# Kernel optimization log

Measured on AMD Instinct MI355X. Metric: run time of the kernel, lower is better.

The kernel has to match this reference:

```python
import jax, jax.numpy as jnp
import numpy as np

N_NODES = 100000
N_EDGES = 1600000
INPUT_DIM = 128
HIDDEN = 128
OUTPUT_DIM = 2
NUM_LAYERS = 2
MAX_RECURSION = 10
TAU_THRESHOLD = 0.005


def setup_inputs() -> dict:
    key = jax.random.key(0)
    ks = jax.random.split(key, 16)
    s = 0.05
    x = jax.random.normal(ks[0], (N_NODES, INPUT_DIM), dtype=jnp.float32)
    edge_index = jax.random.randint(ks[1], (2, N_EDGES), 0, N_NODES, dtype=jnp.int64)
    W_in = jax.random.normal(ks[2], (HIDDEN, INPUT_DIM), dtype=jnp.float32) * s
    b_in = jax.random.normal(ks[3], (HIDDEN,), dtype=jnp.float32) * s
    Wd = jax.random.normal(ks[4], (NUM_LAYERS, HIDDEN, 2 * HIDDEN), dtype=jnp.float32) * s
    bd = jax.random.normal(ks[5], (NUM_LAYERS, HIDDEN), dtype=jnp.float32) * s
    Wt = jax.random.normal(ks[6], (1, HIDDEN), dtype=jnp.float32) * s
    bt = jax.random.normal(ks[7], (1,), dtype=jnp.float32) * s
    W_ih = jax.random.normal(ks[8], (3 * HIDDEN, HIDDEN), dtype=jnp.float32) * s
    W_hh = jax.random.normal(ks[9], (3 * HIDDEN, HIDDEN), dtype=jnp.float32) * s
    b_ih = jax.random.normal(ks[10], (3 * HIDDEN,), dtype=jnp.float32) * s
    b_hh = jax.random.normal(ks[11], (3 * HIDDEN,), dtype=jnp.float32) * s
    Wo = jax.random.normal(ks[12], (OUTPUT_DIM, HIDDEN), dtype=jnp.float32) * s
    bo = jax.random.normal(ks[13], (OUTPUT_DIM,), dtype=jnp.float32) * s
    return dict(x=x, edge_index=edge_index, W_in=W_in, b_in=b_in, Wd=Wd, bd=bd,
                Wt=Wt, bt=bt, W_ih=W_ih, W_hh=W_hh, b_ih=b_ih, b_hh=b_hh, Wo=Wo, bo=bo)


def _gru_cell(x, h, W_ih, W_hh, b_ih, b_hh):
    # torch.nn.GRUCell math
    gi = x @ W_ih.T + b_ih  # [N, 3H]
    gh = h @ W_hh.T + b_hh
    i_r, i_z, i_n = jnp.split(gi, 3, axis=-1)
    h_r, h_z, h_n = jnp.split(gh, 3, axis=-1)
    r = jax.nn.sigmoid(i_r + h_r)
    z = jax.nn.sigmoid(i_z + h_z)
    n = jnp.tanh(i_n + r * h_n)
    return (1.0 - z) * n + z * h


def reference(x, edge_index, W_in, b_in, Wd, bd, Wt, bt, W_ih, W_hh, b_ih, b_hh, Wo, bo):
    N = x.shape[0]
    row, col = edge_index[0], edge_index[1]
    h = jax.nn.relu(x @ W_in.T + b_in)  # [N, H]
    tau = None
    for l in range(NUM_LAYERS):
        diff = jnp.abs(h[row] - h[col])  # [E, H]
        diff_agg = jax.ops.segment_sum(diff, row, num_segments=N)  # [N, H]
        h = jax.nn.relu(jnp.concatenate([h, diff_agg], axis=-1) @ Wd[l].T + bd[l])
        tau = jax.nn.softplus(h @ Wt.T + bt).squeeze(-1)  # [N]
        # n_updates = clamp(floor(1/tau), max=MAX_RECURSION); node updated iff
        # n_updates > 0 and tau < TAU_THRESHOLD. The original inner loop applies
        # gru(diff_agg[i], h[i]) with the ORIGINAL h[i] each iteration, so repeated
        # application is idempotent -> single masked GRU step is exact same math.
        n_updates = jnp.minimum(jnp.floor(1.0 / tau).astype(jnp.int32), MAX_RECURSION)
        mask = (n_updates > 0) & (tau < TAU_THRESHOLD)
        h_gru = _gru_cell(diff_agg, h, W_ih, W_hh, b_ih, b_hh)
        h = jnp.where(mask[:, None], h_gru, h)
    out = h @ Wo.T + bo  # [N, OUTPUT_DIM]
    return out, tau
```

## Files before the change

### kernel.cpp

```cpp
#include <hip/hip_runtime.h>
#include <cstdint>
#include <cstddef>

#define HID 128
#define BSHIFT 7
#define NSB 256

__global__ void transpose_kernel(const float* __restrict__ src, float* __restrict__ dst,
                                 int R, int C) {
  int i = blockIdx.x * blockDim.x + threadIdx.x;
  if (i < R * C) {
    int r = i / C, c = i - r * C;
    dst[c * R + r] = src[i];
  }
}

__global__ __launch_bounds__(256)
void ecount_kernel(const int* __restrict__ row, int* __restrict__ countsT,
                   int E, int nbuck) {
  __shared__ int lh[1024];
  int b = blockIdx.x;
  for (int i = threadIdx.x; i < nbuck; i += 256) lh[i] = 0;
  __syncthreads();
  int per = (E + NSB - 1) / NSB;
  int s = b * per, e = min(s + per, E);
  for (int i = s + (int)threadIdx.x; i < e; i += 256)
    atomicAdd(&lh[row[i] >> BSHIFT], 1);
  __syncthreads();
  for (int i = threadIdx.x; i < nbuck; i += 256) countsT[i * NSB + b] = lh[i];
}

__global__ __launch_bounds__(NSB)
void bprefix_kernel(int* __restrict__ countsT, int* __restrict__ btotal, int nbuck) {
  __shared__ int sd[NSB];
  int bk = blockIdx.x;
  int t = threadIdx.x;
  int v = countsT[bk * NSB + t];
  sd[t] = v;
  __syncthreads();
  for (int off = 1; off < NSB; off <<= 1) {
    int u = (t >= off) ? sd[t - off] : 0;
    __syncthreads();
    sd[t] += u;
    __syncthreads();
  }
  countsT[bk * NSB + t] = sd[t] - v;
  if (t == NSB - 1) btotal[bk] = sd[t];
}

__global__ __launch_bounds__(1024)
void bstart_kernel(const int* __restrict__ btotal, int* __restrict__ bstart,
                   int* __restrict__ offsets, int N, int nbuck) {
  __shared__ int sd[1024];
  int t = threadIdx.x;
  int v = (t < nbuck) ? btotal[t] : 0;
  sd[t] = v;
  __syncthreads();
  for (int off = 1; off < 1024; off <<= 1) {
    int u = (t >= off) ? sd[t - off] : 0;
    __syncthreads();
    sd[t] += u;
    __syncthreads();
  }
  if (t < nbuck) bstart[t] = sd[t] - v;
  if (t == nbuck - 1) { bstart[nbuck] = sd[t]; offsets[N] = sd[t]; }
}

__global__ __launch_bounds__(256)
void escatter_kernel(const int* __restrict__ row, const int* __restrict__ col,
                     const int* __restrict__ countsT, const int* __restrict__ bstart,
                     int2* __restrict__ ebuf, int E, int nbuck) {
  __shared__ int lcur[1024];
  int b = blockIdx.x;
  for (int i = threadIdx.x; i < nbuck; i += 256)
    lcur[i] = bstart[i] + countsT[i * NSB + b];
  __syncthreads();
  int per = (E + NSB - 1) / NSB;
  int s = b * per, e = min(s + per, E);
  for (int i = s + (int)threadIdx.x; i < e; i += 256) {
    int r = row[i], c = col[i];
    int pos = atomicAdd(&lcur[r >> BSHIFT], 1);
    ebuf[pos] = make_int2(r, c);
  }
}

__global__ __launch_bounds__(256)
void bsort_kernel(const int2* __restrict__ ebuf, const int* __restrict__ bstart,
                  int* __restrict__ offsets, int* __restrict__ csr_col,
                  int N, int nbuck) {
  __shared__ int cnt[128], off[128], cur[128];
  int bk = blockIdx.x;
  int tid = threadIdx.x;
  int s = bstart[bk], e = bstart[bk + 1];
  if (tid < 128) cnt[tid] = 0;
  __syncthreads();
  for (int i = s + tid; i < e; i += 256)
    atomicAdd(&cnt[ebuf[i].x & 127], 1);
  __syncthreads();
  if (tid < 128) off[tid] = cnt[tid];
  __syncthreads();
  for (int d = 1; d < 128; d <<= 1) {
    int v = 0;
    if (tid < 128 && tid >= d) v = off[tid - d];
    __syncthreads();
    if (tid < 128) off[tid] += v;
    __syncthreads();
  }
  if (tid < 128) {
    int ex = s + off[tid] - cnt[tid];
    cur[tid] = ex;
    int node = (bk << BSHIFT) + tid;
    if (node < N) offsets[node] = ex;
  }
  __syncthreads();
  for (int i = s + tid; i < e; i += 256) {
    int2 rc = ebuf[i];
    int pos = atomicAdd(&cur[rc.x & 127], 1);
    csr_col[pos] = rc.y;
  }
}

__global__ __launch_bounds__(256)
void aggregate_kernel(const float* __restrict__ h, const int* __restrict__ offsets,
                      const int* __restrict__ csr_col, float* __restrict__ diff,
                      int N) {
  int wave = threadIdx.x >> 6;
  int lane = threadIdx.x & 63;
  int node = blockIdx.x * 4 + wave;
  if (node >= N) return;
  int start = offsets[node], end = offsets[node + 1];
  int deg = end - start;
  const float* hrow = h + (size_t)node * HID;
  float hv0 = hrow[lane], hv1 = hrow[lane + 64];
  float a0 = 0.f, a1 = 0.f;

  int batch = min(deg, 64);
  int myc = (lane < batch) ? csr_col[start + lane] : 0;
  int j = 0;
  for (; j + 8 <= batch; j += 8) {
    const float* p0 = h + (size_t)__shfl(myc, j + 0) * HID;
    const float* p1 = h + (size_t)__shfl(myc, j + 1) * HID;
    const float* p2 = h + (size_t)__shfl(myc, j + 2) * HID;
    const float* p3 = h + (size_t)__shfl(myc, j + 3) * HID;
    const float* p4 = h + (size_t)__shfl(myc, j + 4) * HID;
    const float* p5 = h + (size_t)__shfl(myc, j + 5) * HID;
    const float* p6 = h + (size_t)__shfl(myc, j + 6) * HID;
    const float* p7 = h + (size_t)__shfl(myc, j + 7) * HID;
    float x00 = p0[lane], x01 = p0[lane + 64];
    float x10 = p1[lane], x11 = p1[lane + 64];
    float x20 = p2[lane], x21 = p2[lane + 64];
    float x30 = p3[lane], x31 = p3[lane + 64];
    float x40 = p4[lane], x41 = p4[lane + 64];
    float x50 = p5[lane], x51 = p5[lane + 64];
    float x60 = p6[lane], x61 = p6[lane + 64];
    float x70 = p7[lane], x71 = p7[lane + 64];
    a0 += fabsf(hv0 - x00) + fabsf(hv0 - x10) + fabsf(hv0 - x20) + fabsf(hv0 - x30)
        + fabsf(hv0 - x40) + fabsf(hv0 - x50) + fabsf(hv0 - x60) + fabsf(hv0 - x70);
    a1 += fabsf(hv1 - x01) + fabsf(hv1 - x11) + fabsf(hv1 - x21) + fabsf(hv1 - x31)
        + fabsf(hv1 - x41) + fabsf(hv1 - x51) + fabsf(hv1 - x61) + fabsf(hv1 - x71);
  }
  for (; j < batch; ++j) {
    const float* p = h + (size_t)__shfl(myc, j) * HID;
    a0 += fabsf(hv0 - p[lane]);
    a1 += fabsf(hv1 - p[lane + 64]);
  }
  for (int e = start + 64; e < end; ++e) {
    int c = csr_col[e];
    const float* p = h + (size_t)c * HID;
    a0 += fabsf(hv0 - p[lane]);
    a1 += fabsf(hv1 - p[lane + 64]);
  }
  diff[(size_t)node * HID + lane] = a0;
  diff[(size_t)node * HID + lane + 64] = a1;
}

template<bool TAU>
__global__ __launch_bounds__(512)
void gemm_kernel(const float* __restrict__ A1, const float* __restrict__ A2,
                 const float* __restrict__ BT, const float* __restrict__ bias,
                 float* __restrict__ C, int M, int nchunks,
                 const float* __restrict__ Wt, const float* __restrict__ bt,
                 float* __restrict__ tau_out) {
  __shared__ float As[32][132];
  __shared__ float Bs[32][128];
  __shared__ float taured[128];
  int tid = threadIdx.x;
  int tx = tid & 31;
  int ty = tid >> 5;
  int i0 = blockIdx.x * 128;
  float acc[8][4] = {};

  for (int kc = 0; kc < nchunks; ++kc) {
    const float* A = (kc < 4) ? A1 : A2;
    int ksrc = (kc & 3) * 32;
    int kglob = kc * 32;
    #pragma unroll
    for (int q = 0; q < 2; ++q) {
      int f = q * 512 + tid;
      int i = f >> 3;
      int kq = (f & 7) << 2;
      int ig = i0 + i; if (ig >= M) ig = M - 1;
      float4 v = *(const float4*)(A + (size_t)ig * HID + ksrc + kq);
      As[kq + 0][i] = v.x; As[kq + 1][i] = v.y;
      As[kq + 2][i] = v.z; As[kq + 3][i] = v.w;
    }
    #pragma unroll
    for (int q = 0; q < 2; ++q) {
      int f = q * 512 + tid;
      int k = f >> 5; int c4 = (f & 31) << 2;
      *(float4*)&Bs[k][c4] = *(const float4*)(BT + (size_t)(kglob + k) * HID + c4);
    }
    __syncthreads();
    #pragma unroll
    for (int k = 0; k < 32; ++k) {
      float a[8], b[4];
      const float4* ap = (const float4*)&As[k][ty * 8];
      float4 a0 = ap[0], a1 = ap[1];
      a[0]=a0.x; a[1]=a0.y; a[2]=a0.z; a[3]=a0.w;
      a[4]=a1.x; a[5]=a1.y; a[6]=a1.z; a[7]=a1.w;
      #pragma unroll
      for (int u = 0; u < 4; ++u) b[u] = Bs[k][tx + 32 * u];
      #pragma unroll
      for (int r = 0; r < 8; ++r)
        #pragma unroll
        for (int u = 0; u < 4; ++u)
          acc[r][u] = fmaf(a[r], b[u], acc[r][u]);
    }
    __syncthreads();
  }

  float bias_r[4], wt_r[4];
  #pragma unroll
  for (int u = 0; u < 4; ++u) { bias_r[u] = bias[tx + 32 * u]; wt_r[u] = 0.f; }
  if constexpr (TAU) {
    #pragma unroll
    for (int u = 0; u < 4; ++u) wt_r[u] = Wt[tx + 32 * u];
  }
  #pragma unroll
  for (int r = 0; r < 8; ++r) {
    int row = i0 + ty * 8 + r;
    bool ok = row < M;
    float p = 0.f;
    #pragma unroll
    for (int u = 0; u < 4; ++u) {
      float v = fmaxf(acc[r][u] + bias_r[u], 0.f);
      if (ok) C[(size_t)row * HID + tx + 32 * u] = v;
      p = fmaf(v, wt_r[u], p);
    }
    if constexpr (TAU) {
      p += __shfl_down(p, 16, 32);
      p += __shfl_down(p, 8, 32);
      p += __shfl_down(p, 4, 32);
      p += __shfl_down(p, 2, 32);
      p += __shfl_down(p, 1, 32);
      if (tx == 0) taured[ty * 8 + r] = p;
    }
  }
  if constexpr (TAU) {
    __syncthreads();
    if (tid < 128) {
      int row = i0 + tid;
      if (row < M) {
        float pre = taured[tid] + bt[0];
        float tau = (pre > 20.f) ? pre : log1pf(expf(pre));
        tau_out[row] = tau;
      }
    }
  }
}

__global__ void compact_kernel(const float* __restrict__ tau, int* __restrict__ list,
                               int* __restrict__ count, int N) {
  for (int i = blockIdx.x * blockDim.x + threadIdx.x; i < N; i += gridDim.x * blockDim.x) {
    float t = tau[i];
    if (t < 0.005f && (1.0f / t) < 2147483648.0f) {
      int p = atomicAdd(count, 1);
      list[p] = i;
    }
  }
}

__global__ __launch_bounds__(256)
void gru_kernel(const float* __restrict__ diff, float* __restrict__ h,
                const int* __restrict__ list, const int* __restrict__ count,
                const float* __restrict__ WihT, const float* __restrict__ WhhT,
                const float* __restrict__ b_ih, const float* __restrict__ b_hh) {
  int cnt = *count;
  int base = blockIdx.x * 16;
  if (base >= cnt) return;
  __shared__ float dl[16][HID];
  __shared__ float hl[16][HID];
  __shared__ int ids[16];
  int tid = threadIdx.x;
  if (tid < 16) ids[tid] = (base + tid < cnt) ? list[base + tid] : -1;
  __syncthreads();
  #pragma unroll
  for (int q = 0; q < 8; ++q) {
    int f = q * 256 + tid;
    int r = f >> 7, c = f & 127;
    int id = ids[r];
    int src = (id >= 0) ? id : 0;
    dl[r][c] = diff[(size_t)src * HID + c];
    hl[r][c] = h[(size_t)src * HID + c];
  }
  __syncthreads();
  int tx = tid & 127, ty = tid >> 7;
  float air[8] = {}, aiz[8] = {}, ain[8] = {}, ahr[8] = {}, ahz[8] = {}, ahn[8] = {};
  for (int k = 0; k < HID; ++k) {
    float wir = WihT[k * 384 + tx];
    float wiz = WihT[k * 384 + 128 + tx];
    float win = WihT[k * 384 + 256 + tx];
    float whr = WhhT[k * 384 + tx];
    float whz = WhhT[k * 384 + 128 + tx];
    float whn = WhhT[k * 384 + 256 + tx];
    #pragma unroll
    for (int r = 0; r < 8; ++r) {
      float dk = dl[ty * 8 + r][k];
      float hk = hl[ty * 8 + r][k];
      air[r] = fmaf(dk, wir, air[r]);
      aiz[r] = fmaf(dk, wiz, aiz[r]);
      ain[r] = fmaf(dk, win, ain[r]);
      ahr[r] = fmaf(hk, whr, ahr[r]);
      ahz[r] = fmaf(hk, whz, ahz[r]);
      ahn[r] = fmaf(hk, whn, ahn[r]);
    }
  }
  float bir = b_ih[tx], biz = b_ih[128 + tx], bin = b_ih[256 + tx];
  float bhr = b_hh[tx], bhz = b_hh[128 + tx], bhn = b_hh[256 + tx];
  #pragma unroll
  for (int r = 0; r < 8; ++r) {
    int id = ids[ty * 8 + r];
    if (id < 0) continue;
    float rg = 1.f / (1.f + expf(-((air[r] + bir) + (ahr[r] + bhr))));
    float z  = 1.f / (1.f + expf(-((aiz[r] + biz) + (ahz[r] + bhz))));
    float n  = tanhf((ain[r] + bin) + rg * (ahn[r] + bhn));
    float hv = hl[ty * 8 + r][tx];
    h[(size_t)id * HID + tx] = (1.f - z) * n + z * hv;
  }
}

__global__ void out_kernel(const float* __restrict__ h, const float* __restrict__ Wo,
                           const float* __restrict__ bo, float* __restrict__ out, int N) {
  int g = blockIdx.x * blockDim.x + threadIdx.x;
  int node = g >> 6;
  int lane = threadIdx.x & 63;
  if (node >= N) return;
  float h0 = h[(size_t)node * HID + lane];
  float h1 = h[(size_t)node * HID + 64 + lane];
  float s0 = h0 * Wo[lane] + h1 * Wo[64 + lane];
  float s1 = h0 * Wo[128 + lane] + h1 * Wo[192 + lane];
  for (int d = 32; d; d >>= 1) {
    s0 += __shfl_down(s0, d);
    s1 += __shfl_down(s1, d);
  }
  if (lane == 0) {
    out[(size_t)node * 2 + 0] = s0 + bo[0];
    out[(size_t)node * 2 + 1] = s1 + bo[1];
  }
}

extern "C" void kernel_launch(void* const* d_in, const int* in_sizes, int n_in,
                              void* d_out, int out_size, void* d_ws, size_t ws_size,
                              hipStream_t stream) {
  const float* x    = (const float*)d_in[0];
  const int*   ei   = (const int*)d_in[1];
  const float* W_in = (const float*)d_in[2];
  const float* b_in = (const float*)d_in[3];
  const float* Wd   = (const float*)d_in[4];
  const float* bd   = (const float*)d_in[5];
  const float* Wt   = (const float*)d_in[6];
  const float* bt   = (const float*)d_in[7];
  const float* W_ih = (const float*)d_in[8];
  const float* W_hh = (const float*)d_in[9];
  const float* b_ih = (const float*)d_in[10];
  const float* b_hh = (const float*)d_in[11];
  const float* Wo   = (const float*)d_in[12];
  const float* bo   = (const float*)d_in[13];

  const int N = in_sizes[0] / HID;
  const int E = in_sizes[1] / 2;
  const int* rowp = ei;
  const int* colp = ei + E;
  const int nbuck = (N + (1 << BSHIFT) - 1) >> BSHIFT;

  char* p = (char*)d_ws;
  auto alloc = [&](size_t bytes) { void* r = (void*)p; p += (bytes + 255) & ~(size_t)255; return r; };
  float* hA     = (float*)alloc((size_t)N * HID * 4);
  float* hB     = (float*)alloc((size_t)N * HID * 4);
  float* diff   = (float*)alloc((size_t)N * HID * 4);
  float* WinT   = (float*)alloc(128 * 128 * 4);
  float* WdT0   = (float*)alloc(256 * 128 * 4);
  float* WdT1   = (float*)alloc(256 * 128 * 4);
  float* WihT   = (float*)alloc(128 * 384 * 4);
  float* WhhT   = (float*)alloc(128 * 384 * 4);
  float* tau0   = (float*)alloc((size_t)N * 4);
  int*   list   = (int*)alloc((size_t)N * 4);
  int*   count  = (int*)alloc(256);
  int*   countsT= (int*)alloc((size_t)1024 * NSB * 4);
  int*   btotal = (int*)alloc(1024 * 4);
  int*   bstart = (int*)alloc(1028 * 4);
  int*   offs   = (int*)alloc(((size_t)N + 1) * 4);
  int*   csrcol = (int*)alloc((size_t)E * 4);
  int2*  ebuf   = (int2*)alloc((size_t)E * 8);

  float* out_ptr = (float*)d_out;
  float* tau_out = (float*)d_out + (size_t)N * 2;

  transpose_kernel<<<(128 * 128 + 255) / 256, 256, 0, stream>>>(W_in, WinT, 128, 128);
  transpose_kernel<<<(128 * 256 + 255) / 256, 256, 0, stream>>>(Wd, WdT0, 128, 256);
  transpose_kernel<<<(128 * 256 + 255) / 256, 256, 0, stream>>>(Wd + 128 * 256, WdT1, 128, 256);
  transpose_kernel<<<(384 * 128 + 255) / 256, 256, 0, stream>>>(W_ih, WihT, 384, 128);
  transpose_kernel<<<(384 * 128 + 255) / 256, 256, 0, stream>>>(W_hh, WhhT, 384, 128);

  ecount_kernel<<<NSB, 256, 0, stream>>>(rowp, countsT, E, nbuck);
  bprefix_kernel<<<nbuck, NSB, 0, stream>>>(countsT, btotal, nbuck);
  bstart_kernel<<<1, 1024, 0, stream>>>(btotal, bstart, offs, N, nbuck);
  escatter_kernel<<<NSB, 256, 0, stream>>>(rowp, colp, countsT, bstart, ebuf, E, nbuck);
  bsort_kernel<<<nbuck, 256, 0, stream>>>(ebuf, bstart, offs, csrcol, N, nbuck);

  const int gemm_blocks = (N + 127) / 128;
  const int agg_blocks = (N + 3) / 4;

  gemm_kernel<false><<<gemm_blocks, 512, 0, stream>>>(
      x, nullptr, WinT, b_in, hA, N, 4, nullptr, nullptr, nullptr);

  aggregate_kernel<<<agg_blocks, 256, 0, stream>>>(hA, offs, csrcol, diff, N);
  gemm_kernel<true><<<gemm_blocks, 512, 0, stream>>>(
      hA, diff, WdT0, bd, hB, N, 8, Wt, bt, tau0);
  hipMemsetAsync(count, 0, 4, stream);
  compact_kernel<<<(N + 255) / 256, 256, 0, stream>>>(tau0, list, count, N);
  gru_kernel<<<(N + 15) / 16, 256, 0, stream>>>(diff, hB, list, count, WihT, WhhT, b_ih, b_hh);

  aggregate_kernel<<<agg_blocks, 256, 0, stream>>>(hB, offs, csrcol, diff, N);
  gemm_kernel<true><<<gemm_blocks, 512, 0, stream>>>(
      hB, diff, WdT1, bd + 128, hA, N, 8, Wt, bt, tau_out);
  hipMemsetAsync(count, 0, 4, stream);
  compact_kernel<<<(N + 255) / 256, 256, 0, stream>>>(tau_out, list, count, N);
  gru_kernel<<<(N + 15) / 16, 256, 0, stream>>>(diff, hA, list, count, WihT, WhhT, b_ih, b_hh);

  out_kernel<<<((size_t)N * 64 + 255) / 256, 256, 0, stream>>>(hA, Wo, bo, out_ptr, N);
}
```

Before: 759.8 us.

## Sort CSR neighbors, vectorize gathers, fuse compaction and transposes, enlarge GRU tiles

Sorts each node's neighbor list inside bsort using shared memory, so gathers in the aggregation touch rows in ascending order. The aggregation kernel switches to float2 loads and stores, and the output layout stays consistent with the input. The five weight transposes are merged into one launch. Stream compaction of the tau mask moves into the GEMM epilogue, which removes the per-layer memsets and compact kernels. The GRU kernel now processes 32 rows per 512-thread block. The trade-off is an extra insertion sort, shared memory use in bsort, and atomics in the GEMM tail.

```diff
diff --git a/kernel.cpp b/kernel.cpp
--- a/kernel.cpp
+++ b/kernel.cpp
@@ -5,14 +5,24 @@
 #define HID 128
 #define BSHIFT 7
 #define NSB 256
-
-__global__ void transpose_kernel(const float* __restrict__ src, float* __restrict__ dst,
-                                 int R, int C) {
-  int i = blockIdx.x * blockDim.x + threadIdx.x;
-  if (i < R * C) {
-    int r = i / C, c = i - r * C;
-    dst[c * R + r] = src[i];
-  }
+#define MAXB 4096
+
+__global__ __launch_bounds__(256)
+void transpose_all_kernel(const float* __restrict__ W_in, const float* __restrict__ Wd,
+                          const float* __restrict__ W_ih, const float* __restrict__ W_hh,
+                          float* __restrict__ WinT, float* __restrict__ WdT0,
+                          float* __restrict__ WdT1, float* __restrict__ WihT,
+                          float* __restrict__ WhhT) {
+  int i = blockIdx.x * 256 + threadIdx.x;
+  if (i < 16384) { int r = i >> 7, c = i & 127; WinT[c * 128 + r] = W_in[i]; return; }
+  i -= 16384;
+  if (i < 32768) { int r = i >> 8, c = i & 255; WdT0[c * 128 + r] = Wd[i]; return; }
+  i -= 32768;
+  if (i < 32768) { int r = i >> 8, c = i & 255; WdT1[c * 128 + r] = Wd[32768 + i]; return; }
+  i -= 32768;
+  if (i < 49152) { int r = i >> 7, c = i & 127; WihT[c * 384 + r] = W_ih[i]; return; }
+  i -= 49152;
+  if (i < 49152) { int r = i >> 7, c = i & 127; WhhT[c * 384 + r] = W_hh[i]; }
 }
 
 __global__ __launch_bounds__(256)
@@ -89,9 +99,11 @@
                   int* __restrict__ offsets, int* __restrict__ csr_col,
                   int N, int nbuck) {
   __shared__ int cnt[128], off[128], cur[128];
+  __shared__ int lcol[MAXB];
   int bk = blockIdx.x;
   int tid = threadIdx.x;
   int s = bstart[bk], e = bstart[bk + 1];
+  int m = e - s;
   if (tid < 128) cnt[tid] = 0;
   __syncthreads();
   for (int i = s + tid; i < e; i += 256)
@@ -107,16 +119,35 @@
     __syncthreads();
   }
   if (tid < 128) {
-    int ex = s + off[tid] - cnt[tid];
-    cur[tid] = ex;
+    cur[tid] = off[tid] - cnt[tid];
     int node = (bk << BSHIFT) + tid;
-    if (node < N) offsets[node] = ex;
-  }
-  __syncthreads();
-  for (int i = s + tid; i < e; i += 256) {
-    int2 rc = ebuf[i];
-    int pos = atomicAdd(&cur[rc.x & 127], 1);
-    csr_col[pos] = rc.y;
+    if (node < N) offsets[node] = s + off[tid] - cnt[tid];
+  }
+  __syncthreads();
+  if (m <= MAXB) {
+    for (int i = s + tid; i < e; i += 256) {
+      int2 rc = ebuf[i];
+      int pos = atomicAdd(&cur[rc.x & 127], 1);
+      lcol[pos] = rc.y;
+    }
+    __syncthreads();
+    if (tid < 128) {
+      int b0 = off[tid] - cnt[tid], b1 = off[tid];
+      for (int i = b0 + 1; i < b1; ++i) {
+        int key = lcol[i];
+        int j = i - 1;
+        while (j >= b0 && lcol[j] > key) { lcol[j + 1] = lcol[j]; --j; }
+        lcol[j + 1] = key;
+      }
+    }
+    __syncthreads();
+    for (int i = tid; i < m; i += 256) csr_col[s + i] = lcol[i];
+  } else {
+    for (int i = s + tid; i < e; i += 256) {
+      int2 rc = ebuf[i];
+      int pos = atomicAdd(&cur[rc.x & 127], 1);
+      csr_col[s + pos] = rc.y;
+    }
   }
 }
 
@@ -130,48 +161,42 @@
   if (node >= N) return;
   int start = offsets[node], end = offsets[node + 1];
   int deg = end - start;
-  const float* hrow = h + (size_t)node * HID;
-  float hv0 = hrow[lane], hv1 = hrow[lane + 64];
+  const float2* hrow = (const float2*)(h + (size_t)node * HID);
+  float2 hv = hrow[lane];
   float a0 = 0.f, a1 = 0.f;
 
   int batch = min(deg, 64);
   int myc = (lane < batch) ? csr_col[start + lane] : 0;
   int j = 0;
   for (; j + 8 <= batch; j += 8) {
-    const float* p0 = h + (size_t)__shfl(myc, j + 0) * HID;
-    const float* p1 = h + (size_t)__shfl(myc, j + 1) * HID;
-    const float* p2 = h + (size_t)__shfl(myc, j + 2) * HID;
-    const float* p3 = h + (size_t)__shfl(myc, j + 3) * HID;
-    const float* p4 = h + (size_t)__shfl(myc, j + 4) * HID;
-    const float* p5 = h + (size_t)__shfl(myc, j + 5) * HID;
-    const float* p6 = h + (size_t)__shfl(myc, j + 6) * HID;
-    const float* p7 = h + (size_t)__shfl(myc, j + 7) * HID;
-    float x00 = p0[lane], x01 = p0[lane + 64];
-    float x10 = p1[lane], x11 = p1[lane + 64];
-    float x20 = p2[lane], x21 = p2[lane + 64];
-    float x30 = p3[lane], x31 = p3[lane + 64];
-    float x40 = p4[lane], x41 = p4[lane + 64];
-    float x50 = p5[lane], x51 = p5[lane + 64];
-    float x60 = p6[lane], x61 = p6[lane + 64];
-    float x70 = p7[lane], x71 = p7[lane + 64];
-    a0 += fabsf(hv0 - x00) + fabsf(hv0 - x10) + fabsf(hv0 - x20) + fabsf(hv0 - x30)
-        + fabsf(hv0 - x40) + fabsf(hv0 - x50) + fabsf(hv0 - x60) + fabsf(hv0 - x70);
-    a1 += fabsf(hv1 - x01) + fabsf(hv1 - x11) + fabsf(hv1 - x21) + fabsf(hv1 - x31)
-        + fabsf(hv1 - x41) + fabsf(hv1 - x51) + fabsf(hv1 - x61) + fabsf(hv1 - x71);
+    const float2* p0 = (const float2*)(h + (size_t)__shfl(myc, j + 0) * HID);
+    const float2* p1 = (const float2*)(h + (size_t)__shfl(myc, j + 1) * HID);
+    const float2* p2 = (const float2*)(h + (size_t)__shfl(myc, j + 2) * HID);
+    const float2* p3 = (const float2*)(h + (size_t)__shfl(myc, j + 3) * HID);
+    const float2* p4 = (const float2*)(h + (size_t)__shfl(myc, j + 4) * HID);
+    const float2* p5 = (const float2*)(h + (size_t)__shfl(myc, j + 5) * HID);
+    const float2* p6 = (const float2*)(h + (size_t)__shfl(myc, j + 6) * HID);
+    const float2* p7 = (const float2*)(h + (size_t)__shfl(myc, j + 7) * HID);
+    float2 x0 = p0[lane], x1 = p1[lane], x2 = p2[lane], x3 = p3[lane];
+    float2 x4 = p4[lane], x5 = p5[lane], x6 = p6[lane], x7 = p7[lane];
+    a0 += fabsf(hv.x - x0.x) + fabsf(hv.x - x1.x) + fabsf(hv.x - x2.x) + fabsf(hv.x - x3.x)
+        + fabsf(hv.x - x4.x) + fabsf(hv.x - x5.x) + fabsf(hv.x - x6.x) + fabsf(hv.x - x7.x);
+    a1 += fabsf(hv.y - x0.y) + fabsf(hv.y - x1.y) + fabsf(hv.y - x2.y) + fabsf(hv.y - x3.y)
+        + fabsf(hv.y - x4.y) + fabsf(hv.y - x5.y) + fabsf(hv.y - x6.y) + fabsf(hv.y - x7.y);
   }
   for (; j < batch; ++j) {
-    const float* p = h + (size_t)__shfl(myc, j) * HID;
-    a0 += fabsf(hv0 - p[lane]);
-    a1 += fabsf(hv1 - p[lane + 64]);
+    const float2* p = (const float2*)(h + (size_t)__shfl(myc, j) * HID);
+    float2 x = p[lane];
+    a0 += fabsf(hv.x - x.x);
+    a1 += fabsf(hv.y - x.y);
   }
   for (int e = start + 64; e < end; ++e) {
-    int c = csr_col[e];
-    const float* p = h + (size_t)c * HID;
-    a0 += fabsf(hv0 - p[lane]);
-    a1 += fabsf(hv1 - p[lane + 64]);
-  }
-  diff[(size_t)node * HID + lane] = a0;
-  diff[(size_t)node * HID + lane + 64] = a1;
+    const float2* p = (const float2*)(h + (size_t)csr_col[e] * HID);
+    float2 x = p[lane];
+    a0 += fabsf(hv.x - x.x);
+    a1 += fabsf(hv.y - x.y);
+  }
+  *(float2*)(diff + (size_t)node * HID + 2 * lane) = make_float2(a0, a1);
 }
 
 template<bool TAU>
@@ -180,7 +205,8 @@
                  const float* __restrict__ BT, const float* __restrict__ bias,
                  float* __restrict__ C, int M, int nchunks,
                  const float* __restrict__ Wt, const float* __restrict__ bt,
-                 float* __restrict__ tau_out) {
+                 float* __restrict__ tau_out, int* __restrict__ mlist,
+                 int* __restrict__ mcount) {
   __shared__ float As[32][132];
   __shared__ float Bs[32][128];
   __shared__ float taured[128];
@@ -264,39 +290,32 @@
         float pre = taured[tid] + bt[0];
         float tau = (pre > 20.f) ? pre : log1pf(expf(pre));
         tau_out[row] = tau;
+        if (tau < 0.005f && (1.0f / tau) < 2147483648.0f) {
+          int pos = atomicAdd(mcount, 1);
+          mlist[pos] = row;
+        }
       }
     }
   }
 }
 
-__global__ void compact_kernel(const float* __restrict__ tau, int* __restrict__ list,
-                               int* __restrict__ count, int N) {
-  for (int i = blockIdx.x * blockDim.x + threadIdx.x; i < N; i += gridDim.x * blockDim.x) {
-    float t = tau[i];
-    if (t < 0.005f && (1.0f / t) < 2147483648.0f) {
-      int p = atomicAdd(count, 1);
-      list[p] = i;
-    }
-  }
-}
-
-__global__ __launch_bounds__(256)
+__global__ __launch_bounds__(512)
 void gru_kernel(const float* __restrict__ diff, float* __restrict__ h,
                 const int* __restrict__ list, const int* __restrict__ count,
                 const float* __restrict__ WihT, const float* __restrict__ WhhT,
                 const float* __restrict__ b_ih, const float* __restrict__ b_hh) {
   int cnt = *count;
-  int base = blockIdx.x * 16;
+  int base = blockIdx.x * 32;
   if (base >= cnt) return;
-  __shared__ float dl[16][HID];
-  __shared__ float hl[16][HID];
-  __shared__ int ids[16];
+  __shared__ float dl[32][HID];
+  __shared__ float hl[32][HID];
+  __shared__ int ids[32];
   int tid = threadIdx.x;
-  if (tid < 16) ids[tid] = (base + tid < cnt) ? list[base + tid] : -1;
+  if (tid < 32) ids[tid] = (base + tid < cnt) ? list[base + tid] : -1;
   __syncthreads();
   #pragma unroll
   for (int q = 0; q < 8; ++q) {
-    int f = q * 256 + tid;
+    int f = q * 512 + tid;
     int r = f >> 7, c = f & 127;
     int id = ids[r];
     int src = (id >= 0) ? id : 0;
@@ -406,11 +425,10 @@
   float* out_ptr = (float*)d_out;
   float* tau_out = (float*)d_out + (size_t)N * 2;
 
-  transpose_kernel<<<(128 * 128 + 255) / 256, 256, 0, stream>>>(W_in, WinT, 128, 128);
-  transpose_kernel<<<(128 * 256 + 255) / 256, 256, 0, stream>>>(Wd, WdT0, 128, 256);
-  transpose_kernel<<<(128 * 256 + 255) / 256, 256, 0, stream>>>(Wd + 128 * 256, WdT1, 128, 256);
-  transpose_kernel<<<(384 * 128 + 255) / 256, 256, 0, stream>>>(W_ih, WihT, 384, 128);
-  transpose_kernel<<<(384 * 128 + 255) / 256, 256, 0, stream>>>(W_hh, WhhT, 384, 128);
+  hipMemsetAsync(count, 0, 8, stream);
+
+  transpose_all_kernel<<<(180224 + 255) / 256, 256, 0, stream>>>(
+      W_in, Wd, W_ih, W_hh, WinT, WdT0, WdT1, WihT, WhhT);
 
   ecount_kernel<<<NSB, 256, 0, stream>>>(rowp, countsT, E, nbuck);
   bprefix_kernel<<<nbuck, NSB, 0, stream>>>(countsT, btotal, nbuck);
@@ -420,23 +438,20 @@
 
   const int gemm_blocks = (N + 127) / 128;
   const int agg_blocks = (N + 3) / 4;
+  const int gru_blocks = (N + 31) / 32;
 
   gemm_kernel<false><<<gemm_blocks, 512, 0, stream>>>(
-      x, nullptr, WinT, b_in, hA, N, 4, nullptr, nullptr, nullptr);
+      x, nullptr, WinT, b_in, hA, N, 4, nullptr, nullptr, nullptr, nullptr, nullptr);
 
   aggregate_kernel<<<agg_blocks, 256, 0, stream>>>(hA, offs, csrcol, diff, N);
   gemm_kernel<true><<<gemm_blocks, 512, 0, stream>>>(
-      hA, diff, WdT0, bd, hB, N, 8, Wt, bt, tau0);
-  hipMemsetAsync(count, 0, 4, stream);
-  compact_kernel<<<(N + 255) / 256, 256, 0, stream>>>(tau0, list, count, N);
-  gru_kernel<<<(N + 15) / 16, 256, 0, stream>>>(diff, hB, list, count, WihT, WhhT, b_ih, b_hh);
+      hA, diff, WdT0, bd, hB, N, 8, Wt, bt, tau0, list, count);
+  gru_kernel<<<gru_blocks, 512, 0, stream>>>(diff, hB, list, count, WihT, WhhT, b_ih, b_hh);
 
   aggregate_kernel<<<agg_blocks, 256, 0, stream>>>(hB, offs, csrcol, diff, N);
   gemm_kernel<true><<<gemm_blocks, 512, 0, stream>>>(
-      hB, diff, WdT1, bd + 128, hA, N, 8, Wt, bt, tau_out);
-  hipMemsetAsync(count, 0, 4, stream);
-  compact_kernel<<<(N + 255) / 256, 256, 0, stream>>>(tau_out, list, count, N);
-  gru_kernel<<<(N + 15) / 16, 256, 0, stream>>>(diff, hA, list, count, WihT, WhhT, b_ih, b_hh);
+      hB, diff, WdT1, bd + 128, hA, N, 8, Wt, bt, tau_out, list, count + 1);
+  gru_kernel<<<gru_blocks, 512, 0, stream>>>(diff, hA, list, count + 1, WihT, WhhT, b_ih, b_hh);
 
   out_kernel<<<((size_t)N * 64 + 255) / 256, 256, 0, stream>>>(hA, Wo, bo, out_ptr, N);
 }
```

After: 781.1 us. 2.8% more time.
